# Kernel optimization log

Hardware: AMD Instinct MI355X
Metric: run time of the kernel (lower is better)

## Reference

```python
import jax, jax.numpy as jnp
import numpy as np

N_NODES = 100000
N_EDGES = 3200000
N_GRAPHS = 2000
F_IN, H, N_CLS = 14, 64, 2


def _glorot(key, shape):
    lim = float(np.sqrt(6.0 / (shape[0] + shape[1])))
    return jax.random.uniform(key, shape, jnp.float32, -lim, lim)


def setup_inputs() -> dict:
    key = jax.random.key(0)
    ks = jax.random.split(key, 16)
    x = jax.random.normal(ks[0], (N_NODES, F_IN), jnp.float32)
    edge_index = jax.random.randint(ks[1], (2, N_EDGES), 0, N_NODES, jnp.int64)
    batch = jnp.sort(jax.random.randint(ks[2], (N_NODES,), 0, N_GRAPHS, jnp.int64))
    return {
        "x": x,
        "W1l": _glorot(ks[3], (F_IN, H)), "W1r": _glorot(ks[4], (F_IN, H)), "b1": jnp.zeros((H,), jnp.float32),
        "W2l": _glorot(ks[5], (H, H)), "W2r": _glorot(ks[6], (H, H)), "b2": jnp.zeros((H,), jnp.float32),
        "W3l": _glorot(ks[7], (H, H)), "W3r": _glorot(ks[8], (H, H)), "b3": jnp.zeros((H,), jnp.float32),
        "W4l": _glorot(ks[9], (H, N_CLS)), "W4r": _glorot(ks[10], (H, N_CLS)), "b4": jnp.zeros((N_CLS,), jnp.float32),
        "edge_index": edge_index,
        "batch": batch,
    }


def _sage_conv(x, Wl, Wr, b, src, dst, inv_deg):
    # mean-aggregate neighbor features: messages flow src -> dst (PyG SAGEConv default)
    agg = jax.ops.segment_sum(x[src], dst, num_segments=N_NODES) * inv_deg
    return agg @ Wl + x @ Wr + b


def reference(x, W1l, W1r, b1, W2l, W2r, b2, W3l, W3r, b3, W4l, W4r, b4, edge_index, batch):
    src, dst = edge_index[0], edge_index[1]
    ones = jnp.ones((src.shape[0],), x.dtype)
    deg = jax.ops.segment_sum(ones, dst, num_segments=N_NODES)
    inv_deg = (1.0 / jnp.maximum(deg, 1.0))[:, None]  # [N,1], isolated nodes -> 0 agg

    h = jax.nn.relu(_sage_conv(x, W1l, W1r, b1, src, dst, inv_deg))
    h = jax.nn.relu(_sage_conv(h, W2l, W2r, b2, src, dst, inv_deg))
    h = jax.nn.relu(_sage_conv(h, W3l, W3r, b3, src, dst, inv_deg))
    h = _sage_conv(h, W4l, W4r, b4, src, dst, inv_deg)

    # global_mean_pool over graphs
    gsum = jax.ops.segment_sum(h, batch, num_segments=N_GRAPHS)
    gcnt = jax.ops.segment_sum(jnp.ones((h.shape[0],), h.dtype), batch, num_segments=N_GRAPHS)
    pooled = gsum / jnp.maximum(gcnt, 1.0)[:, None]
    return jax.nn.log_softmax(pooled, axis=-1)
```

## Files before the change

kernel.cpp:

```cpp
#include <hip/hip_runtime.h>
#include <hip/hip_fp16.h>

#define NN 100000
#define NE 3200000
#define NG 2000
#define FIN 14
#define HD 64
#define NC 2

#define NBUK 256
#define BNODES 391
#define P1E 4096
#define BUFCAP 13312

typedef unsigned int uint;

__device__ __forceinline__ __half2 u2h(uint u) {
    union { uint u; __half2 h; } c; c.u = u; return c.h;
}
__device__ __forceinline__ uint h2u(__half2 h) {
    union { __half2 h; uint u; } c; c.h = h; return c.u;
}
__device__ __forceinline__ uint pkh(float a, float b) {
    return h2u(__floats2half2_rn(a, b));
}


__global__ __launch_bounds__(256) void k_hist_bucket(const int* __restrict__ dst,
                                                     int* __restrict__ bkcnt) {
    __shared__ int cnt[NBUK];
    int t = threadIdx.x;
    cnt[t] = 0;
    __syncthreads();
    int e0 = blockIdx.x * P1E;
    int m = NE - e0; if (m > P1E) m = P1E;
    for (int e = t; e < m; e += 256) atomicAdd(&cnt[dst[e0 + e] / BNODES], 1);
    __syncthreads();
    if (cnt[t] > 0) atomicAdd(&bkcnt[t], cnt[t]);
}

__global__ void k_scanb(const int* __restrict__ bkcnt, int* __restrict__ bbase,
                        int* __restrict__ bcur) {
    __shared__ int tmp[NBUK];
    int t = threadIdx.x;
    int v = bkcnt[t];
    tmp[t] = v;
    __syncthreads();
    for (int off = 1; off < NBUK; off <<= 1) {
        int u = (t >= off) ? tmp[t - off] : 0;
        __syncthreads();
        tmp[t] += u;
        __syncthreads();
    }
    int excl = tmp[t] - v;
    bbase[t] = excl;
    bcur[t] = excl;
    if (t == NBUK - 1) bbase[NBUK] = tmp[t];
}

__global__ void k_gbounds(const int* __restrict__ batch, int* __restrict__ gstart,
                          int* __restrict__ gend) {
    int i = blockIdx.x * blockDim.x + threadIdx.x;
    if (i < NN) {
        int b = batch[i];
        if (i == 0 || batch[i - 1] != b) gstart[b] = i;
        if (i == NN - 1 || batch[i + 1] != b) gend[b] = i + 1;
    }
}

__global__ __launch_bounds__(256) void k_pass1(
    const int* __restrict__ src, const int* __restrict__ dst,
    int* __restrict__ bcur, int* __restrict__ pairs) {
    __shared__ int cnt[NBUK];
    __shared__ int scanb[NBUK + 1];
    __shared__ int cur[NBUK];
    __shared__ int gbase[NBUK];
    __shared__ int pbuf[P1E];
    __shared__ unsigned char bsl[P1E];
    int t = threadIdx.x;
    int e0 = blockIdx.x * P1E;
    int m = NE - e0; if (m > P1E) m = P1E;
    cnt[t] = 0;
    __syncthreads();
    int ds[16], ss[16], bk[16];
#pragma unroll
    for (int j = 0; j < 16; ++j) {
        int e = t + j * 256;
        if (e < m) {
            ds[j] = dst[e0 + e];
            ss[j] = src[e0 + e];
            bk[j] = ds[j] / BNODES;
            atomicAdd(&cnt[bk[j]], 1);
        } else bk[j] = -1;
    }
    __syncthreads();
    int v = cnt[t];
    scanb[t] = v;
    __syncthreads();
    for (int off = 1; off < 256; off <<= 1) {
        int u = (t >= off) ? scanb[t - off] : 0;
        __syncthreads();
        scanb[t] += u;
        __syncthreads();
    }
    int excl = scanb[t] - v;
    scanb[t] = excl;
    cur[t] = excl;
    if (t == 255) scanb[256] = excl + v;
    __syncthreads();
#pragma unroll
    for (int j = 0; j < 16; ++j) {
        if (bk[j] >= 0) {
            int p = atomicAdd(&cur[bk[j]], 1);
            pbuf[p] = ss[j] | ((ds[j] - bk[j] * BNODES) << 17);
            bsl[p] = (unsigned char)bk[j];
        }
    }
    int cb = scanb[t + 1] - scanb[t];
    if (cb > 0) gbase[t] = atomicAdd(&bcur[t], cb);
    __syncthreads();
    for (int s = t; s < m; s += 256) {
        int b = bsl[s];
        pairs[gbase[b] + (s - scanb[b])] = pbuf[s];
    }
}

__global__ __launch_bounds__(256) void k_pass2(
    const int* __restrict__ pairs, const int* __restrict__ bbase,
    int* __restrict__ deg, int* __restrict__ rs, int* __restrict__ csr) {
    __shared__ int buf1[BUFCAP];
    __shared__ int buf2[BUFCAP];
    __shared__ int cnt[512];
    __shared__ int rsl[512];
    __shared__ int cur[512];
    __shared__ int s1[256];
    int b = blockIdx.x;
    int n0 = b * BNODES;
    if (n0 >= NN) return;
    int nlocal = NN - n0; if (nlocal > BNODES) nlocal = BNODES;
    int t = threadIdx.x;
    int base = bbase[b];
    int m = bbase[b + 1] - base;
    bool fits = (m <= BUFCAP);
    cnt[t] = 0; cnt[t + 256] = 0;
    __syncthreads();
    for (int s = t; s < m; s += 256) {
        int pk = pairs[base + s];
        if (fits) buf1[s] = pk;
        atomicAdd(&cnt[(uint)pk >> 17], 1);
    }
    __syncthreads();
    int c0 = cnt[2 * t], c1 = cnt[2 * t + 1];
    int ps = c0 + c1;
    s1[t] = ps;
    __syncthreads();
    for (int off = 1; off < 256; off <<= 1) {
        int u = (t >= off) ? s1[t - off] : 0;
        __syncthreads();
        s1[t] += u;
        __syncthreads();
    }
    int pexcl = s1[t] - ps;
    rsl[2 * t] = pexcl;          cur[2 * t] = pexcl;
    rsl[2 * t + 1] = pexcl + c0; cur[2 * t + 1] = pexcl + c0;
    __syncthreads();
    for (int i = t; i < nlocal; i += 256) {
        deg[n0 + i] = cnt[i];
        rs[n0 + i] = base + rsl[i];
    }
    if (fits) {
        for (int s = t; s < m; s += 256) {
            int pk = buf1[s];
            int p = atomicAdd(&cur[(uint)pk >> 17], 1);
            buf2[p] = pk & 0x1FFFF;
        }
        __syncthreads();
        for (int s = t; s < m; s += 256) csr[base + s] = buf2[s];
    } else {
        for (int s = t; s < m; s += 256) {
            int pk = pairs[base + s];
            int p = atomicAdd(&cur[(uint)pk >> 17], 1);
            csr[base + p] = pk & 0x1FFFF;
        }
    }
}


__global__ void k_packx(const float* __restrict__ x, uint* __restrict__ xh) {
    int t = blockIdx.x * blockDim.x + threadIdx.x;
    if (t < NN * 8) {
        int row = t >> 3, q = t & 7;
        int j0 = 2 * q, j1 = 2 * q + 1;
        float f0 = (j0 < FIN) ? x[row * FIN + j0] : 0.f;
        float f1 = (j1 < FIN) ? x[row * FIN + j1] : 0.f;
        xh[t] = pkh(f0, f1);
    }
}


__global__ __launch_bounds__(256, 6) void k_layer1(
    const float* __restrict__ x, const uint* __restrict__ xh, uint* __restrict__ hout,
    const float* __restrict__ Wl, const float* __restrict__ Wr, const float* __restrict__ b,
    const int* __restrict__ rs, const int* __restrict__ deg, const int* __restrict__ csr) {
    __shared__ float2 sW[FIN][HD];
    __shared__ float sb[HD];
    __shared__ float2 sAH[4][16];
    for (int i = threadIdx.x; i < FIN * HD; i += 256) {
        int k = i >> 6, j = i & 63;
        sW[k][j] = make_float2(Wl[i], Wr[i]);
    }
    if (threadIdx.x < HD) sb[threadIdx.x] = b[threadIdx.x];
    __syncthreads();
    int lane = threadIdx.x & 63, wid = threadIdx.x >> 6;
    int sub = lane >> 3;
    int fq = lane & 7;
    int ngroups = (NN + 3) / 4;
    for (int g = blockIdx.x; g < ngroups; g += gridDim.x) {
        int n = g * 4 + wid;
        bool act = n < NN;
        if (act) {
            int s0 = rs[n], d = deg[n];
            float xv = (lane < FIN) ? x[n * FIN + lane] : 0.f;
            __half2 Z = __float2half2_rn(0.f);
            __half2 A0 = Z, A1 = Z, A2 = Z, A3 = Z, A4 = Z, A5 = Z, A6 = Z, A7 = Z;
            for (int base = 0; base < d; base += 64) {
                int rem = d - base; if (rem > 64) rem = 64;
                int idxv = (lane < rem) ? csr[s0 + base + lane] : 0;
                int j = 0;
                for (; j + 64 <= rem; j += 64) {
                    int i0 = __shfl(idxv, j + 0 + sub);
                    int i1 = __shfl(idxv, j + 8 + sub);
                    int i2 = __shfl(idxv, j + 16 + sub);
                    int i3 = __shfl(idxv, j + 24 + sub);
                    int i4 = __shfl(idxv, j + 32 + sub);
                    int i5 = __shfl(idxv, j + 40 + sub);
                    int i6 = __shfl(idxv, j + 48 + sub);
                    int i7 = __shfl(idxv, j + 56 + sub);
                    A0 = __hadd2(A0, u2h(xh[(size_t)i0 * 8 + fq]));
                    A1 = __hadd2(A1, u2h(xh[(size_t)i1 * 8 + fq]));
                    A2 = __hadd2(A2, u2h(xh[(size_t)i2 * 8 + fq]));
                    A3 = __hadd2(A3, u2h(xh[(size_t)i3 * 8 + fq]));
                    A4 = __hadd2(A4, u2h(xh[(size_t)i4 * 8 + fq]));
                    A5 = __hadd2(A5, u2h(xh[(size_t)i5 * 8 + fq]));
                    A6 = __hadd2(A6, u2h(xh[(size_t)i6 * 8 + fq]));
                    A7 = __hadd2(A7, u2h(xh[(size_t)i7 * 8 + fq]));
                }
                for (; j + 8 <= rem; j += 8) {
                    int i0 = __shfl(idxv, j + sub);
                    A0 = __hadd2(A0, u2h(xh[(size_t)i0 * 8 + fq]));
                }
                if (j < rem) {
                    int i0 = __shfl(idxv, j + sub);
                    if (sub < rem - j) A0 = __hadd2(A0, u2h(xh[(size_t)i0 * 8 + fq]));
                }
            }
            A0 = __hadd2(A0, A1); A2 = __hadd2(A2, A3);
            A4 = __hadd2(A4, A5); A6 = __hadd2(A6, A7);
            A0 = __hadd2(A0, A2); A4 = __hadd2(A4, A6);
            A0 = __hadd2(A0, A4);
            float ax = __low2float(A0), ay = __high2float(A0);
            for (int off = 8; off <= 32; off <<= 1) {
                ax += __shfl_xor(ax, off);
                ay += __shfl_xor(ay, off);
            }
            float inv = 1.0f / (float)(d > 1 ? d : 1);
            float e0 = __shfl(ax, lane >> 1);
            float e1 = __shfl(ay, lane >> 1);
            float sel = (lane & 1) ? e1 : e0;
            if (lane < 16) sAH[wid][lane] = make_float2((lane < FIN) ? sel * inv : 0.f, xv);
        }
        float out = sb[lane];
#pragma unroll
        for (int k = 0; k < FIN; ++k) {
            float2 w = sW[k][lane];
            float2 ah = sAH[wid][k];
            out += ah.x * w.x + ah.y * w.y;
        }
        out = fmaxf(out, 0.f);
        float o2 = __shfl_xor(out, 1);
        if (act && !(lane & 1)) hout[(size_t)n * 32 + (lane >> 1)] = pkh(out, o2);
    }
}


template <bool FUSEZ>
__global__ __launch_bounds__(256, 6) void k_layerH(
    const uint* __restrict__ hin, uint* __restrict__ hout,
    const float* __restrict__ Wl, const float* __restrict__ Wr, const float* __restrict__ b,
    const float* __restrict__ W4l, float* __restrict__ z,
    const int* __restrict__ rs, const int* __restrict__ deg, const int* __restrict__ csr) {
    __shared__ uint sWp[HD][HD];
    __shared__ float sb[HD], sW4l[HD * NC];
    __shared__ float2 sAH[4][HD];
    for (int i = threadIdx.x; i < HD * HD; i += 256) {
        int k = i >> 6, j = i & 63;
        sWp[k][j] = pkh(Wl[i], Wr[i]);
    }
    if (threadIdx.x < HD) sb[threadIdx.x] = b[threadIdx.x];
    if (FUSEZ && threadIdx.x < HD * NC) sW4l[threadIdx.x] = W4l[threadIdx.x];
    __syncthreads();
    const uint2* hb2 = (const uint2*)hin;
    int lane = threadIdx.x & 63, wid = threadIdx.x >> 6;
    int sub = lane >> 4;
    int fq = lane & 15;
    int ngroups = (NN + 3) / 4;
    for (int g = blockIdx.x; g < ngroups; g += gridDim.x) {
        int n = g * 4 + wid;
        bool act = n < NN;
        if (act) {
            int s0 = rs[n], d = deg[n];
            __half2 hh = u2h(hin[(size_t)n * 32 + (lane >> 1)]);
            float hv = (lane & 1) ? __high2float(hh) : __low2float(hh);
            __half2 Zh = __float2half2_rn(0.f);
            __half2 P0 = Zh, P1 = Zh, P2 = Zh, P3 = Zh, P4 = Zh, P5 = Zh, P6 = Zh, P7 = Zh;
            __half2 Q0 = Zh, Q1 = Zh, Q2 = Zh, Q3 = Zh, Q4 = Zh, Q5 = Zh, Q6 = Zh, Q7 = Zh;
            for (int base = 0; base < d; base += 64) {
                int rem = d - base; if (rem > 64) rem = 64;
                int idxv = (lane < rem) ? csr[s0 + base + lane] : 0;
                int j = 0;
                for (; j + 32 <= rem; j += 32) {
                    int i0 = __shfl(idxv, j + 0 + sub);
                    int i1 = __shfl(idxv, j + 4 + sub);
                    int i2 = __shfl(idxv, j + 8 + sub);
                    int i3 = __shfl(idxv, j + 12 + sub);
                    int i4 = __shfl(idxv, j + 16 + sub);
                    int i5 = __shfl(idxv, j + 20 + sub);
                    int i6 = __shfl(idxv, j + 24 + sub);
                    int i7 = __shfl(idxv, j + 28 + sub);
                    uint2 U;
                    U = hb2[(size_t)i0 * 16 + fq]; P0 = __hadd2(P0, u2h(U.x)); Q0 = __hadd2(Q0, u2h(U.y));
                    U = hb2[(size_t)i1 * 16 + fq]; P1 = __hadd2(P1, u2h(U.x)); Q1 = __hadd2(Q1, u2h(U.y));
                    U = hb2[(size_t)i2 * 16 + fq]; P2 = __hadd2(P2, u2h(U.x)); Q2 = __hadd2(Q2, u2h(U.y));
                    U = hb2[(size_t)i3 * 16 + fq]; P3 = __hadd2(P3, u2h(U.x)); Q3 = __hadd2(Q3, u2h(U.y));
                    U = hb2[(size_t)i4 * 16 + fq]; P4 = __hadd2(P4, u2h(U.x)); Q4 = __hadd2(Q4, u2h(U.y));
                    U = hb2[(size_t)i5 * 16 + fq]; P5 = __hadd2(P5, u2h(U.x)); Q5 = __hadd2(Q5, u2h(U.y));
                    U = hb2[(size_t)i6 * 16 + fq]; P6 = __hadd2(P6, u2h(U.x)); Q6 = __hadd2(Q6, u2h(U.y));
                    U = hb2[(size_t)i7 * 16 + fq]; P7 = __hadd2(P7, u2h(U.x)); Q7 = __hadd2(Q7, u2h(U.y));
                }
                for (; j + 4 <= rem; j += 4) {
                    int i0 = __shfl(idxv, j + sub);
                    uint2 U = hb2[(size_t)i0 * 16 + fq];
                    P0 = __hadd2(P0, u2h(U.x)); Q0 = __hadd2(Q0, u2h(U.y));
                }
                if (j < rem) {
                    int i0 = __shfl(idxv, j + sub);
                    if (sub < rem - j) {
                        uint2 U = hb2[(size_t)i0 * 16 + fq];
                        P0 = __hadd2(P0, u2h(U.x)); Q0 = __hadd2(Q0, u2h(U.y));
                    }
                }
            }
            P0 = __hadd2(P0, P1); P2 = __hadd2(P2, P3);
            P4 = __hadd2(P4, P5); P6 = __hadd2(P6, P7);
            Q0 = __hadd2(Q0, Q1); Q2 = __hadd2(Q2, Q3);
            Q4 = __hadd2(Q4, Q5); Q6 = __hadd2(Q6, Q7);
            P0 = __hadd2(P0, P2); P4 = __hadd2(P4, P6);
            Q0 = __hadd2(Q0, Q2); Q4 = __hadd2(Q4, Q6);
            P0 = __hadd2(P0, P4); Q0 = __hadd2(Q0, Q4);
            float4 A0 = make_float4(__low2float(P0), __high2float(P0),
                                    __low2float(Q0), __high2float(Q0));
            for (int off = 16; off <= 32; off <<= 1) {
                A0.x += __shfl_xor(A0.x, off);
                A0.y += __shfl_xor(A0.y, off);
                A0.z += __shfl_xor(A0.z, off);
                A0.w += __shfl_xor(A0.w, off);
            }
            float inv = 1.0f / (float)(d > 1 ? d : 1);
            A0.x *= inv; A0.y *= inv; A0.z *= inv; A0.w *= inv;
            float e0 = __shfl(A0.x, lane >> 2);
            float e1 = __shfl(A0.y, lane >> 2);
            float e2 = __shfl(A0.z, lane >> 2);
            float e3 = __shfl(A0.w, lane >> 2);
            int c = lane & 3;
            float sel = (c == 0) ? e0 : (c == 1) ? e1 : (c == 2) ? e2 : e3;
            sAH[wid][lane] = make_float2(sel, hv);
        }
        float out = sb[lane];
#pragma unroll 8
        for (int k = 0; k < HD; ++k) {
            __half2 wh = u2h(sWp[k][lane]);
            float2 ah = sAH[wid][k];
            out += ah.x * __low2float(wh) + ah.y * __high2float(wh);
        }
        out = fmaxf(out, 0.f);
        float o2 = __shfl_xor(out, 1);
        if (act && !(lane & 1)) hout[(size_t)n * 32 + (lane >> 1)] = pkh(out, o2);
        if (FUSEZ) {
            float r0 = out * sW4l[lane * NC + 0];
            float r1 = out * sW4l[lane * NC + 1];
            for (int off = 32; off; off >>= 1) {
                r0 += __shfl_xor(r0, off);
                r1 += __shfl_xor(r1, off);
            }
            if (act && lane == 0) ((float2*)z)[n] = make_float2(r0, r1);
        }
    }
}


__global__ __launch_bounds__(256) void k_pool(
    const uint* __restrict__ h3, const float* __restrict__ z,
    const float* __restrict__ W4r, const float* __restrict__ b4,
    const int* __restrict__ rs, const int* __restrict__ deg, const int* __restrict__ csr,
    const int* __restrict__ batch, float* __restrict__ gsum) {
    __shared__ float sW[HD * NC];
    if (threadIdx.x < HD * NC) sW[threadIdx.x] = W4r[threadIdx.x];
    __syncthreads();
    const float2* z2 = (const float2*)z;
    int lane = threadIdx.x & 63, wid = threadIdx.x >> 6;
    int stride = gridDim.x * 4;
    for (int n = blockIdx.x * 4 + wid; n < NN; n += stride) {
        float r0 = 0.f, r1 = 0.f;
        if (lane < 32) {
            __half2 h = u2h(h3[(size_t)n * 32 + lane]);
            float f0 = __low2float(h), f1 = __high2float(h);
            r0 = f0 * sW[(2 * lane) * NC + 0] + f1 * sW[(2 * lane + 1) * NC + 0];
            r1 = f0 * sW[(2 * lane) * NC + 1] + f1 * sW[(2 * lane + 1) * NC + 1];
        }
        int s0 = rs[n], d = deg[n];
        float a0 = 0.f, a1 = 0.f;
        for (int j = lane; j < d; j += 64) {
            int s = csr[s0 + j];
            float2 zv = z2[s];
            a0 += zv.x;
            a1 += zv.y;
        }
        for (int off = 32; off; off >>= 1) {
            r0 += __shfl_xor(r0, off);
            r1 += __shfl_xor(r1, off);
            a0 += __shfl_xor(a0, off);
            a1 += __shfl_xor(a1, off);
        }
        if (lane == 0) {
            float inv = 1.0f / (float)(d > 1 ? d : 1);
            float o0 = a0 * inv + r0 + b4[0];
            float o1 = a1 * inv + r1 + b4[1];
            int gg = batch[n];
            atomicAdd(&gsum[gg * 2 + 0], o0);
            atomicAdd(&gsum[gg * 2 + 1], o1);
        }
    }
}

__global__ void k_final(const float* __restrict__ gsum, const int* __restrict__ gstart,
                        const int* __restrict__ gend, float* __restrict__ out) {
    int g = blockIdx.x * blockDim.x + threadIdx.x;
    if (g < NG) {
        int cnt = gend[g] - gstart[g];
        float inv = 1.0f / (float)(cnt > 1 ? cnt : 1);
        float p0 = gsum[g * 2 + 0] * inv;
        float p1 = gsum[g * 2 + 1] * inv;
        float m = fmaxf(p0, p1);
        float lse = m + logf(expf(p0 - m) + expf(p1 - m));
        out[g * 2 + 0] = p0 - lse;
        out[g * 2 + 1] = p1 - lse;
    }
}


extern "C" void kernel_launch(void* const* d_in, const int* in_sizes, int n_in,
                              void* d_out, int out_size, void* d_ws, size_t ws_size,
                              hipStream_t stream) {
    const float* x   = (const float*)d_in[0];
    const float* W1l = (const float*)d_in[1];
    const float* W1r = (const float*)d_in[2];
    const float* b1  = (const float*)d_in[3];
    const float* W2l = (const float*)d_in[4];
    const float* W2r = (const float*)d_in[5];
    const float* b2  = (const float*)d_in[6];
    const float* W3l = (const float*)d_in[7];
    const float* W3r = (const float*)d_in[8];
    const float* b3  = (const float*)d_in[9];
    const float* W4l = (const float*)d_in[10];
    const float* W4r = (const float*)d_in[11];
    const float* b4  = (const float*)d_in[12];
    const int* ei    = (const int*)d_in[13];
    const int* batch = (const int*)d_in[14];
    const int* src = ei;
    const int* dst = ei + NE;
    float* out = (float*)d_out;

    char* w = (char*)d_ws;
    int* deg    = (int*)w; w += (size_t)NN * 4;
    int* rs     = (int*)w; w += (size_t)NN * 4;
    int* csr    = (int*)w; w += (size_t)NE * 4;
    int* gstart = (int*)w; w += (size_t)NG * 4;
    int* gend   = (int*)w; w += (size_t)NG * 4;
    int* bkcnt  = (int*)w; w += NBUK * 4;
    int* bbase  = (int*)w; w += (NBUK + 1) * 4;
    int* bcur   = (int*)w; w += NBUK * 4;
    w = (char*)(((uintptr_t)w + 255) & ~(uintptr_t)255);
    uint* xh    = (uint*)w; w += (size_t)NN * 8 * 4;
    uint* hA    = (uint*)w; w += (size_t)NN * 32 * 4;
    uint* hB    = (uint*)w; w += (size_t)NN * 32 * 4;
    float* z    = (float*)w; w += (size_t)NN * NC * 4;
    float* gsum = (float*)w; w += (size_t)NG * NC * 4;
    int* pairs = (int*)hB;

    const int P1B = (NE + P1E - 1) / P1E;

    hipMemsetAsync(bkcnt, 0, NBUK * 4, stream);
    hipMemsetAsync(gstart, 0, (size_t)NG * 4, stream);
    hipMemsetAsync(gend, 0, (size_t)NG * 4, stream);
    hipMemsetAsync(gsum, 0, (size_t)NG * NC * 4, stream);

    k_hist_bucket<<<P1B, 256, 0, stream>>>(dst, bkcnt);
    k_packx<<<(NN * 8 + 255) / 256, 256, 0, stream>>>(x, xh);
    k_gbounds<<<(NN + 255) / 256, 256, 0, stream>>>(batch, gstart, gend);
    k_scanb<<<1, NBUK, 0, stream>>>(bkcnt, bbase, bcur);
    k_pass1<<<P1B, 256, 0, stream>>>(src, dst, bcur, pairs);
    k_pass2<<<NBUK, 256, 0, stream>>>(pairs, bbase, deg, rs, csr);

    k_layer1<<<1536, 256, 0, stream>>>(x, xh, hA, W1l, W1r, b1, rs, deg, csr);
    k_layerH<false><<<1536, 256, 0, stream>>>(hA, hB, W2l, W2r, b2, nullptr, nullptr, rs, deg, csr);
    k_layerH<true><<<1536, 256, 0, stream>>>(hB, hA, W3l, W3r, b3, W4l, z, rs, deg, csr);
    k_pool<<<2048, 256, 0, stream>>>(hA, z, W4r, b4, rs, deg, csr, batch, gsum);
    k_final<<<(NG + 255) / 256, 256, 0, stream>>>(gsum, gstart, gend, out);
}
```

Before: 444.2 us.

## Use bf16 MFMA for hidden-layer dense transform over 16-node tiles

```diff
diff --git a/kernel.cpp b/kernel.cpp
--- a/kernel.cpp
+++ b/kernel.cpp
@@ -13,7 +13,14 @@
 #define P1E 4096
 #define BUFCAP 13312
 
+#define AHU 68
+#define WCH 136
+#define NGB ((NN + 63) / 64)
+
 typedef unsigned int uint;
+typedef short short8 __attribute__((ext_vector_type(8)));
+typedef float f32x4 __attribute__((ext_vector_type(4)));
+union U128 { uint4 u; short8 s; };
 
 __device__ __forceinline__ __half2 u2h(uint u) {
     union { uint u; __half2 h; } c; c.u = u; return c.h;
@@ -23,6 +30,16 @@
 }
 __device__ __forceinline__ uint pkh(float a, float b) {
     return h2u(__floats2half2_rn(a, b));
+}
+__device__ __forceinline__ uint pack2bf16(float a, float b) {
+    uint ua = __float_as_uint(a), ub = __float_as_uint(b);
+    ua = (ua + 0x7FFFu + ((ua >> 16) & 1u)) >> 16;
+    ub = (ub + 0x7FFFu + ((ub >> 16) & 1u)) >> 16;
+    return ua | (ub << 16);
+}
+__device__ __forceinline__ unsigned short bf16of(float a) {
+    uint ua = __float_as_uint(a);
+    return (unsigned short)((ua + 0x7FFFu + ((ua >> 16) & 1u)) >> 16);
 }
 
 
@@ -284,33 +301,32 @@
 
 
 template <bool FUSEZ>
-__global__ __launch_bounds__(256, 6) void k_layerH(
+__global__ __launch_bounds__(256, 4) void k_layerH(
     const uint* __restrict__ hin, uint* __restrict__ hout,
     const float* __restrict__ Wl, const float* __restrict__ Wr, const float* __restrict__ b,
     const float* __restrict__ W4l, float* __restrict__ z,
     const int* __restrict__ rs, const int* __restrict__ deg, const int* __restrict__ csr) {
-    __shared__ uint sWp[HD][HD];
+    __shared__ uint sAHb[4][16 * AHU];
+    __shared__ unsigned short sWT[64 * WCH];
     __shared__ float sb[HD], sW4l[HD * NC];
-    __shared__ float2 sAH[4][HD];
-    for (int i = threadIdx.x; i < HD * HD; i += 256) {
-        int k = i >> 6, j = i & 63;
-        sWp[k][j] = pkh(Wl[i], Wr[i]);
+    for (int i = threadIdx.x; i < 64 * 128; i += 256) {
+        int j = i >> 7, kk = i & 127;
+        float v = (kk < 64) ? Wl[kk * 64 + j] : Wr[(kk - 64) * 64 + j];
+        sWT[j * WCH + kk] = bf16of(v);
     }
     if (threadIdx.x < HD) sb[threadIdx.x] = b[threadIdx.x];
     if (FUSEZ && threadIdx.x < HD * NC) sW4l[threadIdx.x] = W4l[threadIdx.x];
     __syncthreads();
-    const uint2* hb2 = (const uint2*)hin;
     int lane = threadIdx.x & 63, wid = threadIdx.x >> 6;
+    uint* AH = sAHb[wid];
     int sub = lane >> 4;
     int fq = lane & 15;
-    int ngroups = (NN + 3) / 4;
-    for (int g = blockIdx.x; g < ngroups; g += gridDim.x) {
-        int n = g * 4 + wid;
-        bool act = n < NN;
-        if (act) {
+    const uint2* hb2 = (const uint2*)hin;
+    int n0 = (blockIdx.x * 4 + wid) * 16;
+    for (int i = 0; i < 16; ++i) {
+        int n = n0 + i;
+        if (n < NN) {
             int s0 = rs[n], d = deg[n];
-            __half2 hh = u2h(hin[(size_t)n * 32 + (lane >> 1)]);
-            float hv = (lane & 1) ? __high2float(hh) : __low2float(hh);
             __half2 Zh = __float2half2_rn(0.f);
             __half2 P0 = Zh, P1 = Zh, P2 = Zh, P3 = Zh, P4 = Zh, P5 = Zh, P6 = Zh, P7 = Zh;
             __half2 Q0 = Zh, Q1 = Zh, Q2 = Zh, Q3 = Zh, Q4 = Zh, Q5 = Zh, Q6 = Zh, Q7 = Zh;
@@ -357,42 +373,79 @@
             P0 = __hadd2(P0, P2); P4 = __hadd2(P4, P6);
             Q0 = __hadd2(Q0, Q2); Q4 = __hadd2(Q4, Q6);
             P0 = __hadd2(P0, P4); Q0 = __hadd2(Q0, Q4);
-            float4 A0 = make_float4(__low2float(P0), __high2float(P0),
-                                    __low2float(Q0), __high2float(Q0));
+            float ax = __low2float(P0), ay = __high2float(P0);
+            float az = __low2float(Q0), aw = __high2float(Q0);
             for (int off = 16; off <= 32; off <<= 1) {
-                A0.x += __shfl_xor(A0.x, off);
-                A0.y += __shfl_xor(A0.y, off);
-                A0.z += __shfl_xor(A0.z, off);
-                A0.w += __shfl_xor(A0.w, off);
+                ax += __shfl_xor(ax, off);
+                ay += __shfl_xor(ay, off);
+                az += __shfl_xor(az, off);
+                aw += __shfl_xor(aw, off);
             }
             float inv = 1.0f / (float)(d > 1 ? d : 1);
-            A0.x *= inv; A0.y *= inv; A0.z *= inv; A0.w *= inv;
-            float e0 = __shfl(A0.x, lane >> 2);
-            float e1 = __shfl(A0.y, lane >> 2);
-            float e2 = __shfl(A0.z, lane >> 2);
-            float e3 = __shfl(A0.w, lane >> 2);
-            int c = lane & 3;
-            float sel = (c == 0) ? e0 : (c == 1) ? e1 : (c == 2) ? e2 : e3;
-            sAH[wid][lane] = make_float2(sel, hv);
-        }
-        float out = sb[lane];
-#pragma unroll 8
-        for (int k = 0; k < HD; ++k) {
-            __half2 wh = u2h(sWp[k][lane]);
-            float2 ah = sAH[wid][k];
-            out += ah.x * __low2float(wh) + ah.y * __high2float(wh);
-        }
-        out = fmaxf(out, 0.f);
-        float o2 = __shfl_xor(out, 1);
-        if (act && !(lane & 1)) hout[(size_t)n * 32 + (lane >> 1)] = pkh(out, o2);
+            ax *= inv; ay *= inv; az *= inv; aw *= inv;
+            if (lane < 16) {
+                AH[i * AHU + 2 * fq] = pack2bf16(ax, ay);
+                AH[i * AHU + 2 * fq + 1] = pack2bf16(az, aw);
+            }
+            if (lane < 32) {
+                __half2 hh = u2h(hin[(size_t)n * 32 + lane]);
+                AH[i * AHU + 32 + lane] = pack2bf16(__low2float(hh), __high2float(hh));
+            }
+        } else {
+            if (lane < 32) { AH[i * AHU + lane] = 0; AH[i * AHU + 32 + lane] = 0; }
+        }
+    }
+    int r16 = lane & 15, qg = lane >> 4;
+    short8 afr[4];
+#pragma unroll
+    for (int c = 0; c < 4; ++c) {
+        U128 a;
+        a.u = *(const uint4*)&AH[r16 * AHU + 16 * c + 4 * qg];
+        afr[c] = a.s;
+    }
+    f32x4 acc[4];
+#pragma unroll
+    for (int t = 0; t < 4; ++t) {
+        float bv = sb[16 * t + r16];
+        acc[t] = (f32x4){bv, bv, bv, bv};
+    }
+#pragma unroll
+    for (int t = 0; t < 4; ++t) {
+#pragma unroll
+        for (int c = 0; c < 4; ++c) {
+            U128 bf;
+            bf.u = *(const uint4*)(sWT + (16 * t + r16) * WCH + 32 * c + 8 * qg);
+            acc[t] = __builtin_amdgcn_mfma_f32_16x16x32_bf16(afr[c], bf.s, acc[t], 0, 0, 0);
+        }
+    }
+    float rz0[4] = {0.f, 0.f, 0.f, 0.f}, rz1[4] = {0.f, 0.f, 0.f, 0.f};
+#pragma unroll
+    for (int t = 0; t < 4; ++t) {
+        float wz0 = 0.f, wz1 = 0.f;
         if (FUSEZ) {
-            float r0 = out * sW4l[lane * NC + 0];
-            float r1 = out * sW4l[lane * NC + 1];
-            for (int off = 32; off; off >>= 1) {
-                r0 += __shfl_xor(r0, off);
-                r1 += __shfl_xor(r1, off);
-            }
-            if (act && lane == 0) ((float2*)z)[n] = make_float2(r0, r1);
+            wz0 = sW4l[(16 * t + r16) * NC + 0];
+            wz1 = sW4l[(16 * t + r16) * NC + 1];
+        }
+#pragma unroll
+        for (int r = 0; r < 4; ++r) {
+            int m = n0 + qg * 4 + r;
+            float out = fmaxf(acc[t][r], 0.f);
+            float o2 = __shfl_xor(out, 1);
+            if (!(lane & 1) && m < NN)
+                hout[(size_t)m * 32 + 8 * t + (r16 >> 1)] = pkh(out, o2);
+            if (FUSEZ) { rz0[r] += out * wz0; rz1[r] += out * wz1; }
+        }
+    }
+    if (FUSEZ) {
+#pragma unroll
+        for (int r = 0; r < 4; ++r) {
+            float a0 = rz0[r], a1 = rz1[r];
+            for (int off = 1; off < 16; off <<= 1) {
+                a0 += __shfl_xor(a0, off);
+                a1 += __shfl_xor(a1, off);
+            }
+            int m = n0 + qg * 4 + r;
+            if (r16 == 0 && m < NN) ((float2*)z)[m] = make_float2(a0, a1);
         }
     }
 }
@@ -512,8 +565,8 @@
     k_pass2<<<NBUK, 256, 0, stream>>>(pairs, bbase, deg, rs, csr);
 
     k_layer1<<<1536, 256, 0, stream>>>(x, xh, hA, W1l, W1r, b1, rs, deg, csr);
-    k_layerH<false><<<1536, 256, 0, stream>>>(hA, hB, W2l, W2r, b2, nullptr, nullptr, rs, deg, csr);
-    k_layerH<true><<<1536, 256, 0, stream>>>(hB, hA, W3l, W3r, b3, W4l, z, rs, deg, csr);
+    k_layerH<false><<<NGB, 256, 0, stream>>>(hA, hB, W2l, W2r, b2, nullptr, nullptr, rs, deg, csr);
+    k_layerH<true><<<NGB, 256, 0, stream>>>(hB, hA, W3l, W3r, b3, W4l, z, rs, deg, csr);
     k_pool<<<2048, 256, 0, stream>>>(hA, z, W4r, b4, rs, deg, csr, batch, gsum);
     k_final<<<(NG + 255) / 256, 256, 0, stream>>>(gsum, gstart, gend, out);
 }
```

Measured after the change: 525.7 us. 18.3% more time.
